# Kernel tuning notes

Measured on AMD Instinct MI355X. Metric: run time of the kernel, lower is better.

The kernel has to match this reference:

```python
import jax, jax.numpy as jnp
import numpy as np
import math

D_K = 64
ROUNDS = 4
BUCKET_LEN = 64


def _l2norm(x, axis):
    n = jnp.sqrt(jnp.sum(x * x, axis=axis, keepdims=True))
    return x / jnp.maximum(n, 1e-12)


def _look_back(x):
    # x: (B, n_buckets, bucket_len, ...) -> (B, n_buckets, 2*bucket_len, ...)
    # each bucket is concatenated with the previous bucket (wrapping at 0)
    shift = jnp.concatenate([x[:, -1:], x[:, :-1]], axis=1)
    return jnp.concatenate([shift, x], axis=2)


def _lsh_hash(query, rand_matrix):
    # returns position-tagged hashes: bucket_id * L + position, shape (B, L, R)
    B, L, D = query.shape
    qn = _l2norm(query, -1)
    rm = _l2norm(rand_matrix, 1)  # normalize over d_k dim, as in torch code
    xR = jnp.einsum('bld,bdrn->blrn', qn, rm)
    h = jnp.argmax(jnp.concatenate([xR, -xR], axis=-1), axis=-1).astype(jnp.int32)
    return h * L + jnp.arange(L, dtype=jnp.int32)[None, :, None]


def _attend(query, value, hash_indice, original_indice, sorted_hashes):
    B, L, D = query.shape
    nb = L // BUCKET_LEN
    R = ROUNDS
    # gather queries into hash-sorted order, per round: (B, L, D, R)
    rq = jnp.take_along_axis(query[:, :, :, None], hash_indice[:, :, None, :], axis=1)
    rq = rq.reshape(B, nb, BUCKET_LEN, D, R)
    lk = _l2norm(_look_back(rq), -2)  # keys = normalized lookback queries (shared QK)
    qk = jnp.einsum('bnijk,bnljk->bnilk', rq, lk) / math.sqrt(D_K)  # (B,nb,bl,2bl,R)
    # mask cross-bucket pairs
    sh = (sorted_hashes // L).reshape(B, nb, BUCKET_LEN, R)
    qk = jnp.where(sh[..., None, :] != _look_back(sh)[..., None, :, :], -1e9, qk)
    # mask self-attention (causal=False so no causal mask)
    qi = hash_indice.reshape(B, nb, BUCKET_LEN, R).astype(jnp.int32)
    ki = _look_back(qi)
    qk = jnp.where(qi[..., None, :] == ki[..., None, :, :], -1e5, qk)
    qk = qk.reshape(B, L, 2 * BUCKET_LEN, R)
    lse = jax.scipy.special.logsumexp(qk, axis=2)  # (B, L, R)
    p = jnp.exp(qk - lse[:, :, None, :]).reshape(B, nb, BUCKET_LEN, 2 * BUCKET_LEN, R)
    # gather values into sorted order and apply lookback attention
    rv = jnp.take_along_axis(value[:, :, :, None], hash_indice[:, :, None, :], axis=1)
    rv = rv.reshape(B, nb, BUCKET_LEN, D, R)
    att = jnp.einsum('bnijl,bnjkl->bnikl', p, _look_back(rv)).reshape(B, L, D, R)
    # scatter back to original order
    att = jnp.take_along_axis(att, original_indice[:, :, None, :], axis=1)
    lse = jnp.take_along_axis(lse, original_indice, axis=1)
    # NOTE: faithful to source, softmax over dim=1 (sequence dim)
    w = jax.nn.softmax(lse, axis=1)  # (B, L, R)
    return jnp.einsum('blir,blr->bli', att, w)  # (B, L, D)


def setup_inputs() -> dict:
    key = jax.random.key(0)
    k1, k2, k3 = jax.random.split(key, 3)
    B, L, D = 16, 8192, D_K
    n_buckets = L // BUCKET_LEN
    return {
        'query': jax.random.normal(k1, (B, L, D), jnp.float32),
        'value': jax.random.normal(k2, (B, L, D), jnp.float32),
        'rand_matrix': jax.random.normal(k3, (B, D, ROUNDS, n_buckets // 2), jnp.float32),
    }


def reference(query, value, rand_matrix):
    hashes = _lsh_hash(query, rand_matrix)          # (B, L, R) int32
    hash_indice = jnp.argsort(hashes, axis=1)       # sort positions by hash
    sorted_hashes = jnp.take_along_axis(hashes, hash_indice, axis=1)
    original_indice = jnp.argsort(hash_indice, axis=1)  # inverse permutation
    return _attend(query, value, hash_indice.astype(jnp.int32),
                   original_indice.astype(jnp.int32), sorted_hashes)
```

## Files before the change

kernel.cpp:

```cpp
#include <hip/hip_runtime.h>
#include <math.h>

#define B_   16
#define L_   8192
#define D_   64
#define R_   4
#define NB_  128
#define NH_  64

__device__ __forceinline__ float dpp_xor1(float x) {
    return __int_as_float(__builtin_amdgcn_mov_dpp(__float_as_int(x), 0xB1, 0xf, 0xf, true));
}
__device__ __forceinline__ float dpp_xor2(float x) {
    return __int_as_float(__builtin_amdgcn_mov_dpp(__float_as_int(x), 0x4E, 0xf, 0xf, true));
}
__device__ __forceinline__ float quad_bcast0(float x) {
    return __int_as_float(__builtin_amdgcn_mov_dpp(__float_as_int(x), 0x00, 0xf, 0xf, true));
}
__device__ __forceinline__ float quad_bcast1(float x) {
    return __int_as_float(__builtin_amdgcn_mov_dpp(__float_as_int(x), 0x55, 0xf, 0xf, true));
}
__device__ __forceinline__ float quad_bcast2(float x) {
    return __int_as_float(__builtin_amdgcn_mov_dpp(__float_as_int(x), 0xAA, 0xf, 0xf, true));
}
__device__ __forceinline__ float quad_bcast3(float x) {
    return __int_as_float(__builtin_amdgcn_mov_dpp(__float_as_int(x), 0xFF, 0xf, 0xf, true));
}

__global__ __launch_bounds__(64) void k_rmnorm(const float* __restrict__ rm, double* __restrict__ rmn) {
    int b = blockIdx.x >> 2, r = blockIdx.x & 3;
    int n = threadIdx.x;
    float v[D_];
    double ss = 0.0;
    #pragma unroll
    for (int d = 0; d < D_; ++d) {
        float f = rm[((size_t)(b * D_ + d) * R_ + r) * NH_ + n];
        v[d] = f;
        ss += (double)f * (double)f;
    }
    double nrm = sqrt(ss); if (nrm < 1e-12) nrm = 1e-12;
    double inv = 1.0 / nrm;
    double* o = rmn + ((size_t)(b * R_ + r) * NH_ + n) * D_;
    #pragma unroll
    for (int d = 0; d < D_; ++d) o[d] = (double)v[d] * inv;
}

__global__ __launch_bounds__(256) void k_hash(const float* __restrict__ q, const double* __restrict__ rmn,
                                              float* __restrict__ rn, int* __restrict__ h) {
    __shared__ double rms[NH_ * D_];
    int b = blockIdx.z, r = blockIdx.y;
    int l = blockIdx.x * 256 + threadIdx.x;
    const double* src = rmn + (size_t)(b * R_ + r) * NH_ * D_;
    for (int i = threadIdx.x; i < NH_ * D_; i += 256) rms[i] = src[i];
    const float* qp = q + ((size_t)b * L_ + l) * D_;
    double qd[D_];
    double ss = 0.0;
    #pragma unroll
    for (int d = 0; d < D_; d += 4) {
        float4 f = *(const float4*)(qp + d);
        qd[d] = f.x; qd[d+1] = f.y; qd[d+2] = f.z; qd[d+3] = f.w;
        ss += (double)f.x * f.x + (double)f.y * f.y + (double)f.z * f.z + (double)f.w * f.w;
    }
    __syncthreads();
    double best = -1.0e300; int bi = 0;
    for (int n = 0; n < NH_; ++n) {
        const double* kp = &rms[n * D_];
        double a0 = 0, a1 = 0, a2 = 0, a3 = 0;
        #pragma unroll
        for (int d = 0; d < D_; d += 4) {
            a0 = fma(qd[d],   kp[d],   a0);
            a1 = fma(qd[d+1], kp[d+1], a1);
            a2 = fma(qd[d+2], kp[d+2], a2);
            a3 = fma(qd[d+3], kp[d+3], a3);
        }
        double s = (a0 + a1) + (a2 + a3);
        if (s > best)  { best = s;  bi = n; }
        if (-s > best) { best = -s; bi = n + NH_; }
    }
    h[(size_t)(b * R_ + r) * L_ + l] = bi;
    if (r == 0) {
        double nrm = sqrt(ss); if (nrm < 1e-12) nrm = 1e-12;
        rn[(size_t)b * L_ + l] = (float)(1.0 / nrm);
    }
}

__global__ __launch_bounds__(64) void k_sort(const int* __restrict__ h, int* __restrict__ idx,
                                             int* __restrict__ sb, int* __restrict__ iv) {
    __shared__ unsigned int cnt[NB_ * 64];
    int br = blockIdx.x;
    const int* hh = h + (size_t)br * L_;
    int t = threadIdx.x;
    for (int i = t; i < NB_ * 64; i += 64) cnt[i] = 0;
    __syncthreads();
    int base = t * 128;
    for (int i = 0; i < 128; ++i) { int bk = hh[base + i]; cnt[bk * 64 + t]++; }
    __syncthreads();
    int fb = t * 128;
    unsigned int local = 0;
    for (int i = 0; i < 128; ++i) local += cnt[fb + i];
    unsigned int v = local;
    #pragma unroll
    for (int off = 1; off < 64; off <<= 1) {
        unsigned int u = __shfl_up(v, off);
        if (t >= off) v += u;
    }
    unsigned int run = v - local;
    for (int i = 0; i < 128; ++i) { unsigned int c0 = cnt[fb + i]; cnt[fb + i] = run; run += c0; }
    __syncthreads();
    int* oi = idx + (size_t)br * L_;
    int* ob = sb  + (size_t)br * L_;
    int* ivp = iv + (size_t)br * L_;
    for (int i = 0; i < 128; ++i) {
        int l = base + i; int bk = hh[l];
        unsigned int pos = cnt[bk * 64 + t]++;
        oi[pos] = l; ob[pos] = bk; ivp[l] = (int)pos;
    }
}

__global__ __launch_bounds__(64, 2) void k_flash(const float* __restrict__ q, const float* __restrict__ val,
                                                 const int* __restrict__ idx, const int* __restrict__ sb,
                                                 const float* __restrict__ rn, float* __restrict__ lse,
                                                 const float* __restrict__ gm, const float* __restrict__ gs,
                                                 float* __restrict__ out, float* __restrict__ contrib,
                                                 int r_fixed, int omode) {
    __shared__ float kt[16 * 80];
    __shared__ float vt[16 * 80];
    __shared__ int   kqs[16];
    __shared__ int   kbs[16];
    __shared__ float krs[16];
    int c = blockIdx.x, b = blockIdx.z;
    int r = (r_fixed < 0) ? (int)blockIdx.y : r_fixed;
    size_t sbase = (size_t)(b * R_ + r) * L_;
    int tid = threadIdx.x;
    int h = tid & 3;
    int posq = c * 64 + (tid >> 2) * 4;
    int mls[4];
    #pragma unroll
    for (int qq = 0; qq < 4; ++qq) mls[qq] = idx[sbase + posq + qq];
    int ownpos  = posq + h;
    int myl_own = idx[sbase + ownpos];
    int mybk_own = sb[sbase + ownpos];
    const float* qb = q   + (size_t)b * L_ * D_;
    const float* vb = val + (size_t)b * L_ * D_;
    float qv[4][16];
    #pragma unroll
    for (int qq = 0; qq < 4; ++qq) {
        const float* qp = qb + (size_t)mls[qq] * D_ + h * 16;
        #pragma unroll
        for (int i = 0; i < 16; i += 4) {
            float4 f = *(const float4*)(qp + i);
            qv[qq][i] = f.x; qv[qq][i+1] = f.y; qv[qq][i+2] = f.z; qv[qq][i+3] = f.w;
        }
    }
    float m = -3.0e38f, sum = 0.0f;
    float acc[4][16];
    #pragma unroll
    for (int qq = 0; qq < 4; ++qq)
        #pragma unroll
        for (int i = 0; i < 16; ++i) acc[qq][i] = 0.0f;

    #pragma unroll 1
    for (int s = 0; s < 8; ++s) {
        int ck = ((c + NB_ - 1 + (s >> 2)) & (NB_ - 1)) * 64 + (s & 3) * 16;
        __syncthreads();
        {
            int rw = tid >> 2, cc = tid & 3;
            int kl = idx[sbase + ck + rw];
            const float* kp = qb + (size_t)kl * D_ + cc * 16;
            float* kd = &kt[rw * 80 + cc * 20];
            #pragma unroll
            for (int i = 0; i < 16; i += 4) *(float4*)(kd + i) = *(const float4*)(kp + i);
            if (omode != 2) {
                const float* vp = vb + (size_t)kl * D_ + cc * 16;
                float* vd = &vt[rw * 80 + cc * 20];
                #pragma unroll
                for (int i = 0; i < 16; i += 4) *(float4*)(vd + i) = *(const float4*)(vp + i);
            }
            if (tid < 16) {
                int kl2 = idx[sbase + ck + tid];
                kqs[tid] = kl2;
                kbs[tid] = sb[sbase + ck + tid];
                krs[tid] = rn[(size_t)b * L_ + kl2];
            }
        }
        __syncthreads();
        float sc[16];
        #pragma unroll
        for (int j = 0; j < 16; ++j) {
            const float* kpj = &kt[j * 80 + h * 20];
            float p0 = 0, p1 = 0, p2 = 0, p3 = 0;
            #pragma unroll
            for (int i = 0; i < 16; i += 4) {
                float4 kk = *(const float4*)(kpj + i);
                p0 = fmaf(qv[0][i], kk.x, p0); p0 = fmaf(qv[0][i+1], kk.y, p0);
                p0 = fmaf(qv[0][i+2], kk.z, p0); p0 = fmaf(qv[0][i+3], kk.w, p0);
                p1 = fmaf(qv[1][i], kk.x, p1); p1 = fmaf(qv[1][i+1], kk.y, p1);
                p1 = fmaf(qv[1][i+2], kk.z, p1); p1 = fmaf(qv[1][i+3], kk.w, p1);
                p2 = fmaf(qv[2][i], kk.x, p2); p2 = fmaf(qv[2][i+1], kk.y, p2);
                p2 = fmaf(qv[2][i+2], kk.z, p2); p2 = fmaf(qv[2][i+3], kk.w, p2);
                p3 = fmaf(qv[3][i], kk.x, p3); p3 = fmaf(qv[3][i+1], kk.y, p3);
                p3 = fmaf(qv[3][i+2], kk.z, p3); p3 = fmaf(qv[3][i+3], kk.w, p3);
            }
            bool b0 = (h & 1), b1 = (h & 2) != 0;
            float u0 = b0 ? p1 : p0;
            float t0 = b0 ? p0 : p1;
            u0 += dpp_xor1(t0);
            float u2 = b0 ? p3 : p2;
            float t2 = b0 ? p2 : p3;
            u2 += dpp_xor1(t2);
            float dot = b1 ? u2 : u0;
            float t3 = b1 ? u0 : u2;
            dot += dpp_xor2(t3);
            float v2 = dot * krs[j] * 0.125f;
            v2 = (kbs[j] == mybk_own) ? v2 : -1.0e9f;
            if (kqs[j] == myl_own) v2 = -1.0e5f;
            sc[j] = v2;
        }
        float M = sc[0];
        #pragma unroll
        for (int j = 1; j < 16; ++j) M = fmaxf(M, sc[j]);
        float mn = fmaxf(m, M);
        float alpha = expf(m - mn);
        float ps = 0.0f;
        #pragma unroll
        for (int j = 0; j < 16; ++j) { sc[j] = expf(sc[j] - mn); ps += sc[j]; }
        sum = fmaf(sum, alpha, ps);
        m = mn;
        if (omode != 2) {
            float al0 = quad_bcast0(alpha), al1 = quad_bcast1(alpha);
            float al2 = quad_bcast2(alpha), al3 = quad_bcast3(alpha);
            #pragma unroll
            for (int i = 0; i < 16; ++i) {
                acc[0][i] *= al0; acc[1][i] *= al1; acc[2][i] *= al2; acc[3][i] *= al3;
            }
            #pragma unroll
            for (int j = 0; j < 16; ++j) {
                float pq0 = quad_bcast0(sc[j]), pq1 = quad_bcast1(sc[j]);
                float pq2 = quad_bcast2(sc[j]), pq3 = quad_bcast3(sc[j]);
                const float* vpj = &vt[j * 80 + h * 20];
                #pragma unroll
                for (int i = 0; i < 16; i += 4) {
                    float4 vv = *(const float4*)(vpj + i);
                    acc[0][i]   = fmaf(pq0, vv.x, acc[0][i]);   acc[0][i+1] = fmaf(pq0, vv.y, acc[0][i+1]);
                    acc[0][i+2] = fmaf(pq0, vv.z, acc[0][i+2]); acc[0][i+3] = fmaf(pq0, vv.w, acc[0][i+3]);
                    acc[1][i]   = fmaf(pq1, vv.x, acc[1][i]);   acc[1][i+1] = fmaf(pq1, vv.y, acc[1][i+1]);
                    acc[1][i+2] = fmaf(pq1, vv.z, acc[1][i+2]); acc[1][i+3] = fmaf(pq1, vv.w, acc[1][i+3]);
                    acc[2][i]   = fmaf(pq2, vv.x, acc[2][i]);   acc[2][i+1] = fmaf(pq2, vv.y, acc[2][i+1]);
                    acc[2][i+2] = fmaf(pq2, vv.z, acc[2][i+2]); acc[2][i+3] = fmaf(pq2, vv.w, acc[2][i+3]);
                    acc[3][i]   = fmaf(pq3, vv.x, acc[3][i]);   acc[3][i+1] = fmaf(pq3, vv.y, acc[3][i+1]);
                    acc[3][i+2] = fmaf(pq3, vv.z, acc[3][i+2]); acc[3][i+3] = fmaf(pq3, vv.w, acc[3][i+3]);
                }
            }
        }
    }
    float lse_own = m + logf(sum);
    if (omode != 3) lse[sbase + ownpos] = lse_own;
    if (omode == 0 || omode == 1) {
        float s0 = quad_bcast0(sum), s1 = quad_bcast1(sum), s2 = quad_bcast2(sum), s3 = quad_bcast3(sum);
        float iv0 = 1.0f / s0, iv1 = 1.0f / s1, iv2 = 1.0f / s2, iv3 = 1.0f / s3;
        float ivs[4] = {iv0, iv1, iv2, iv3};
        float* cbase = contrib + ((omode == 0) ? (size_t)(b * R_ + r) * L_ : (size_t)b * L_) * D_;
        #pragma unroll
        for (int qq = 0; qq < 4; ++qq) {
            float* cp = cbase + (size_t)(posq + qq) * D_ + h * 16;
            #pragma unroll
            for (int i = 0; i < 16; i += 4) {
                float4 o;
                o.x = acc[qq][i] * ivs[qq];   o.y = acc[qq][i+1] * ivs[qq];
                o.z = acc[qq][i+2] * ivs[qq]; o.w = acc[qq][i+3] * ivs[qq];
                *(float4*)(cp + i) = o;
            }
        }
    } else if (omode == 3) {
        int brr = b * R_ + r;
        float gmv = gm[brr], gsv = gs[brr];
        float l0 = quad_bcast0(lse_own), l1 = quad_bcast1(lse_own);
        float l2 = quad_bcast2(lse_own), l3 = quad_bcast3(lse_own);
        float s0 = quad_bcast0(sum), s1 = quad_bcast1(sum), s2 = quad_bcast2(sum), s3 = quad_bcast3(sum);
        float ws[4];
        ws[0] = expf(l0 - gmv) * gsv / s0; ws[1] = expf(l1 - gmv) * gsv / s1;
        ws[2] = expf(l2 - gmv) * gsv / s2; ws[3] = expf(l3 - gmv) * gsv / s3;
        #pragma unroll
        for (int qq = 0; qq < 4; ++qq) {
            float* op = out + ((size_t)b * L_ + mls[qq]) * D_ + h * 16;
            #pragma unroll
            for (int i = 0; i < 16; ++i) unsafeAtomicAdd(op + i, ws[qq] * acc[qq][i]);
        }
    }
}

__global__ __launch_bounds__(256) void k_wred(const float* __restrict__ lse, float* __restrict__ gm,
                                              float* __restrict__ gs, int r_w) {
    __shared__ float  sm[4];
    __shared__ double sd[4];
    int br = (r_w < 0) ? (int)blockIdx.x : ((int)blockIdx.x * R_ + r_w);
    const float* x = lse + (size_t)br * L_;
    int t = threadIdx.x;
    float mx = -3.0e38f;
    for (int i = t; i < L_; i += 256) mx = fmaxf(mx, x[i]);
    #pragma unroll
    for (int o = 32; o; o >>= 1) mx = fmaxf(mx, __shfl_down(mx, o));
    if ((t & 63) == 0) sm[t >> 6] = mx;
    __syncthreads();
    mx = fmaxf(fmaxf(sm[0], sm[1]), fmaxf(sm[2], sm[3]));
    double s = 0.0;
    for (int i = t; i < L_; i += 256) s += exp((double)x[i] - (double)mx);
    #pragma unroll
    for (int o = 32; o; o >>= 1) s += __shfl_down(s, o);
    if ((t & 63) == 0) sd[t >> 6] = s;
    __syncthreads();
    if (t == 0) { gm[br] = mx; gs[br] = (float)(1.0 / (sd[0] + sd[1] + sd[2] + sd[3])); }
}

__global__ __launch_bounds__(256) void k_comb_full(const float* __restrict__ contrib,
                                                   const int* __restrict__ iv,
                                                   const float* __restrict__ lse,
                                                   const float* __restrict__ gm,
                                                   const float* __restrict__ gs,
                                                   float* __restrict__ out) {
    int gid = blockIdx.x * 256 + threadIdx.x;
    int row = gid >> 2;
    int ch  = (gid & 3) * 16;
    int b = row >> 13, l = row & (L_ - 1);
    float s[16];
    #pragma unroll
    for (int i = 0; i < 16; ++i) s[i] = 0.0f;
    #pragma unroll
    for (int r = 0; r < R_; ++r) {
        int brr = b * R_ + r;
        int pos = iv[(size_t)brr * L_ + l];
        float w = expf(lse[(size_t)brr * L_ + pos] - gm[brr]) * gs[brr];
        const float* cp = contrib + ((size_t)brr * L_ + pos) * D_ + ch;
        #pragma unroll
        for (int i = 0; i < 16; i += 4) {
            float4 f = *(const float4*)(cp + i);
            s[i]   = fmaf(w, f.x, s[i]);   s[i+1] = fmaf(w, f.y, s[i+1]);
            s[i+2] = fmaf(w, f.z, s[i+2]); s[i+3] = fmaf(w, f.w, s[i+3]);
        }
    }
    float* op = out + (size_t)row * D_ + ch;
    #pragma unroll
    for (int i = 0; i < 16; i += 4) {
        float4 o; o.x = s[i]; o.y = s[i+1]; o.z = s[i+2]; o.w = s[i+3];
        *(float4*)(op + i) = o;
    }
}

__global__ __launch_bounds__(256) void k_comb_add(const float* __restrict__ contrib,
                                                  const int* __restrict__ iv,
                                                  const float* __restrict__ lse,
                                                  const float* __restrict__ gm,
                                                  const float* __restrict__ gs,
                                                  float* __restrict__ out, int r) {
    int gid = blockIdx.x * 256 + threadIdx.x;
    int row = gid >> 2;
    int ch  = (gid & 3) * 16;
    int b = row >> 13, l = row & (L_ - 1);
    int brr = b * R_ + r;
    int pos = iv[(size_t)brr * L_ + l];
    float w = expf(lse[(size_t)brr * L_ + pos] - gm[brr]) * gs[brr];
    const float* cp = contrib + ((size_t)b * L_ + pos) * D_ + ch;
    float* op = out + (size_t)row * D_ + ch;
    #pragma unroll
    for (int i = 0; i < 16; i += 4) {
        float4 f = *(const float4*)(cp + i);
        float4 o = *(const float4*)(op + i);
        o.x = fmaf(w, f.x, o.x); o.y = fmaf(w, f.y, o.y);
        o.z = fmaf(w, f.z, o.z); o.w = fmaf(w, f.w, o.w);
        *(float4*)(op + i) = o;
    }
}

#define OFF_RMN     0u
#define OFF_RN      2097152u
#define OFF_H       2621440u
#define OFF_IDX     4718592u
#define OFF_SB      6815744u
#define OFF_LSE     8912896u
#define OFF_GM      11010048u
#define OFF_GS      11010304u
#define OFF_INV     11010560u
#define OFF_CONTRIB 13107712u
#define CONTRIB_FULL_BYTES  134217728ull
#define CONTRIB_SLICE_BYTES 33554432ull

extern "C" void kernel_launch(void* const* d_in, const int* in_sizes, int n_in,
                              void* d_out, int out_size, void* d_ws, size_t ws_size,
                              hipStream_t stream) {
    const float* q  = (const float*)d_in[0];
    const float* v  = (const float*)d_in[1];
    const float* rm = (const float*)d_in[2];
    float* out = (float*)d_out;
    char* ws = (char*)d_ws;
    double* rmn = (double*)(ws + OFF_RMN);
    float*  rn  = (float*)(ws + OFF_RN);
    int*    h   = (int*)(ws + OFF_H);
    int*    idx = (int*)(ws + OFF_IDX);
    int*    sb  = (int*)(ws + OFF_SB);
    float*  lse = (float*)(ws + OFF_LSE);
    float*  gm  = (float*)(ws + OFF_GM);
    float*  gs  = (float*)(ws + OFF_GS);
    int*    iv  = (int*)(ws + OFF_INV);
    float*  contrib = (float*)(ws + OFF_CONTRIB);

    int tierA = (ws_size >= (size_t)OFF_CONTRIB + CONTRIB_FULL_BYTES) ? 1 : 0;
    int tierB = (!tierA && ws_size >= (size_t)OFF_CONTRIB + CONTRIB_SLICE_BYTES) ? 1 : 0;

    hipLaunchKernelGGL(k_rmnorm, dim3(B_ * R_), dim3(64), 0, stream, rm, rmn);
    hipLaunchKernelGGL(k_hash, dim3(L_ / 256, R_, B_), dim3(256), 0, stream, q, rmn, rn, h);
    hipLaunchKernelGGL(k_sort, dim3(B_ * R_), dim3(64), 0, stream, h, idx, sb, iv);

    if (tierA) {
        hipLaunchKernelGGL(k_flash, dim3(NB_, R_, B_), dim3(64), 0, stream, q, v, idx, sb, rn,
                           lse, gm, gs, out, contrib, -1, 0);
        hipLaunchKernelGGL(k_wred, dim3(B_ * R_), dim3(256), 0, stream, lse, gm, gs, -1);
        hipLaunchKernelGGL(k_comb_full, dim3(B_ * L_ * 4 / 256), dim3(256), 0, stream,
                           contrib, iv, lse, gm, gs, out);
    } else if (tierB) {
        hipMemsetAsync(d_out, 0, (size_t)B_ * L_ * D_ * sizeof(float), stream);
        for (int r = 0; r < R_; ++r) {
            hipLaunchKernelGGL(k_flash, dim3(NB_, 1, B_), dim3(64), 0, stream, q, v, idx, sb, rn,
                               lse, gm, gs, out, contrib, r, 1);
            hipLaunchKernelGGL(k_wred, dim3(B_), dim3(256), 0, stream, lse, gm, gs, r);
            hipLaunchKernelGGL(k_comb_add, dim3(B_ * L_ * 4 / 256), dim3(256), 0, stream,
                               contrib, iv, lse, gm, gs, out, r);
        }
    } else {
        hipMemsetAsync(d_out, 0, (size_t)B_ * L_ * D_ * sizeof(float), stream);
        hipLaunchKernelGGL(k_flash, dim3(NB_, R_, B_), dim3(64), 0, stream, q, v, idx, sb, rn,
                           lse, gm, gs, out, contrib, -1, 2);
        hipLaunchKernelGGL(k_wred, dim3(B_ * R_), dim3(256), 0, stream, lse, gm, gs, -1);
        hipLaunchKernelGGL(k_flash, dim3(NB_, R_, B_), dim3(64), 0, stream, q, v, idx, sb, rn,
                           lse, gm, gs, out, contrib, -1, 3);
    }
}
```

Measured before the change: 648.1 us.

## Use fp32 hashing with fp64 fallback and fixed-max softmax in attention

```diff
diff --git a/kernel.cpp b/kernel.cpp
--- a/kernel.cpp
+++ b/kernel.cpp
@@ -47,35 +47,64 @@
 
 __global__ __launch_bounds__(256) void k_hash(const float* __restrict__ q, const double* __restrict__ rmn,
                                               float* __restrict__ rn, int* __restrict__ h) {
-    __shared__ double rms[NH_ * D_];
+    __shared__ double rmd[NH_ * D_];
+    __shared__ float  rms[NH_ * D_];
     int b = blockIdx.z, r = blockIdx.y;
     int l = blockIdx.x * 256 + threadIdx.x;
     const double* src = rmn + (size_t)(b * R_ + r) * NH_ * D_;
-    for (int i = threadIdx.x; i < NH_ * D_; i += 256) rms[i] = src[i];
+    for (int i = threadIdx.x; i < NH_ * D_; i += 256) {
+        double dv = src[i];
+        rmd[i] = dv;
+        rms[i] = (float)dv;
+    }
     const float* qp = q + ((size_t)b * L_ + l) * D_;
-    double qd[D_];
+    float qf[D_];
     double ss = 0.0;
     #pragma unroll
     for (int d = 0; d < D_; d += 4) {
         float4 f = *(const float4*)(qp + d);
-        qd[d] = f.x; qd[d+1] = f.y; qd[d+2] = f.z; qd[d+3] = f.w;
+        qf[d] = f.x; qf[d+1] = f.y; qf[d+2] = f.z; qf[d+3] = f.w;
         ss += (double)f.x * f.x + (double)f.y * f.y + (double)f.z * f.z + (double)f.w * f.w;
     }
     __syncthreads();
-    double best = -1.0e300; int bi = 0;
+    float best = -1.0e30f, second = -1.0e30f; int bi = 0;
     for (int n = 0; n < NH_; ++n) {
-        const double* kp = &rms[n * D_];
-        double a0 = 0, a1 = 0, a2 = 0, a3 = 0;
+        const float* kp = &rms[n * D_];
+        float a0 = 0, a1 = 0, a2 = 0, a3 = 0;
         #pragma unroll
         for (int d = 0; d < D_; d += 4) {
-            a0 = fma(qd[d],   kp[d],   a0);
-            a1 = fma(qd[d+1], kp[d+1], a1);
-            a2 = fma(qd[d+2], kp[d+2], a2);
-            a3 = fma(qd[d+3], kp[d+3], a3);
-        }
-        double s = (a0 + a1) + (a2 + a3);
-        if (s > best)  { best = s;  bi = n; }
-        if (-s > best) { best = -s; bi = n + NH_; }
+            a0 = fmaf(qf[d],   kp[d],   a0);
+            a1 = fmaf(qf[d+1], kp[d+1], a1);
+            a2 = fmaf(qf[d+2], kp[d+2], a2);
+            a3 = fmaf(qf[d+3], kp[d+3], a3);
+        }
+        float s = (a0 + a1) + (a2 + a3);
+        if (s > best)       { second = best; best = s; bi = n; }
+        else if (s > second)  second = s;
+        float ns = -s;
+        if (ns > best)      { second = best; best = ns; bi = n + NH_; }
+        else if (ns > second) second = ns;
+    }
+    float qn = (float)sqrt(ss);
+    if (best - second < 3.0e-5f * qn + 1.0e-7f) {
+        double qd[D_];
+        #pragma unroll
+        for (int d = 0; d < D_; ++d) qd[d] = (double)qf[d];
+        double bestd = -1.0e300; bi = 0;
+        for (int n = 0; n < NH_; ++n) {
+            const double* kp = &rmd[n * D_];
+            double a0 = 0, a1 = 0, a2 = 0, a3 = 0;
+            #pragma unroll
+            for (int d = 0; d < D_; d += 4) {
+                a0 = fma(qd[d],   kp[d],   a0);
+                a1 = fma(qd[d+1], kp[d+1], a1);
+                a2 = fma(qd[d+2], kp[d+2], a2);
+                a3 = fma(qd[d+3], kp[d+3], a3);
+            }
+            double s = (a0 + a1) + (a2 + a3);
+            if (s > bestd)  { bestd = s;  bi = n; }
+            if (-s > bestd) { bestd = -s; bi = n + NH_; }
+        }
     }
     h[(size_t)(b * R_ + r) * L_ + l] = bi;
     if (r == 0) {
@@ -140,6 +169,7 @@
     int ownpos  = posq + h;
     int myl_own = idx[sbase + ownpos];
     int mybk_own = sb[sbase + ownpos];
+    float m_own = 0.125f / rn[(size_t)b * L_ + myl_own];
     const float* qb = q   + (size_t)b * L_ * D_;
     const float* vb = val + (size_t)b * L_ * D_;
     float qv[4][16];
@@ -152,7 +182,7 @@
             qv[qq][i] = f.x; qv[qq][i+1] = f.y; qv[qq][i+2] = f.z; qv[qq][i+3] = f.w;
         }
     }
-    float m = -3.0e38f, sum = 0.0f;
+    float ps[4] = {0.0f, 0.0f, 0.0f, 0.0f};
     float acc[4][16];
     #pragma unroll
     for (int qq = 0; qq < 4; ++qq)
@@ -180,11 +210,10 @@
                 int kl2 = idx[sbase + ck + tid];
                 kqs[tid] = kl2;
                 kbs[tid] = sb[sbase + ck + tid];
-                krs[tid] = rn[(size_t)b * L_ + kl2];
+                krs[tid] = rn[(size_t)b * L_ + kl2] * 0.125f;
             }
         }
         __syncthreads();
-        float sc[16];
         #pragma unroll
         for (int j = 0; j < 16; ++j) {
             const float* kpj = &kt[j * 80 + h * 20];
@@ -211,32 +240,14 @@
             float dot = b1 ? u2 : u0;
             float t3 = b1 ? u0 : u2;
             dot += dpp_xor2(t3);
-            float v2 = dot * krs[j] * 0.125f;
-            v2 = (kbs[j] == mybk_own) ? v2 : -1.0e9f;
-            if (kqs[j] == myl_own) v2 = -1.0e5f;
-            sc[j] = v2;
-        }
-        float M = sc[0];
-        #pragma unroll
-        for (int j = 1; j < 16; ++j) M = fmaxf(M, sc[j]);
-        float mn = fmaxf(m, M);
-        float alpha = expf(m - mn);
-        float ps = 0.0f;
-        #pragma unroll
-        for (int j = 0; j < 16; ++j) { sc[j] = expf(sc[j] - mn); ps += sc[j]; }
-        sum = fmaf(sum, alpha, ps);
-        m = mn;
-        if (omode != 2) {
-            float al0 = quad_bcast0(alpha), al1 = quad_bcast1(alpha);
-            float al2 = quad_bcast2(alpha), al3 = quad_bcast3(alpha);
-            #pragma unroll
-            for (int i = 0; i < 16; ++i) {
-                acc[0][i] *= al0; acc[1][i] *= al1; acc[2][i] *= al2; acc[3][i] *= al3;
-            }
-            #pragma unroll
-            for (int j = 0; j < 16; ++j) {
-                float pq0 = quad_bcast0(sc[j]), pq1 = quad_bcast1(sc[j]);
-                float pq2 = quad_bcast2(sc[j]), pq3 = quad_bcast3(sc[j]);
+            float sc = dot * krs[j];
+            sc = (kbs[j] == mybk_own) ? sc : -1.0e9f;
+            if (kqs[j] == myl_own) sc = -1.0e5f;
+            float p = __expf(sc - m_own);
+            ps[j & 3] += p;
+            if (omode != 2) {
+                float pq0 = quad_bcast0(p), pq1 = quad_bcast1(p);
+                float pq2 = quad_bcast2(p), pq3 = quad_bcast3(p);
                 const float* vpj = &vt[j * 80 + h * 20];
                 #pragma unroll
                 for (int i = 0; i < 16; i += 4) {
@@ -253,12 +264,15 @@
             }
         }
     }
-    float lse_own = m + logf(sum);
+    float sum = (ps[0] + ps[1]) + (ps[2] + ps[3]);
+    float lse_own, inv_own;
+    if (sum > 0.0f) { lse_own = m_own + logf(sum); inv_own = 1.0f / sum; }
+    else            { lse_own = -3.0e38f;          inv_own = 0.0f; }
     if (omode != 3) lse[sbase + ownpos] = lse_own;
     if (omode == 0 || omode == 1) {
-        float s0 = quad_bcast0(sum), s1 = quad_bcast1(sum), s2 = quad_bcast2(sum), s3 = quad_bcast3(sum);
-        float iv0 = 1.0f / s0, iv1 = 1.0f / s1, iv2 = 1.0f / s2, iv3 = 1.0f / s3;
-        float ivs[4] = {iv0, iv1, iv2, iv3};
+        float ivs[4];
+        ivs[0] = quad_bcast0(inv_own); ivs[1] = quad_bcast1(inv_own);
+        ivs[2] = quad_bcast2(inv_own); ivs[3] = quad_bcast3(inv_own);
         float* cbase = contrib + ((omode == 0) ? (size_t)(b * R_ + r) * L_ : (size_t)b * L_) * D_;
         #pragma unroll
         for (int qq = 0; qq < 4; ++qq) {
@@ -274,17 +288,17 @@
     } else if (omode == 3) {
         int brr = b * R_ + r;
         float gmv = gm[brr], gsv = gs[brr];
-        float l0 = quad_bcast0(lse_own), l1 = quad_bcast1(lse_own);
-        float l2 = quad_bcast2(lse_own), l3 = quad_bcast3(lse_own);
-        float s0 = quad_bcast0(sum), s1 = quad_bcast1(sum), s2 = quad_bcast2(sum), s3 = quad_bcast3(sum);
-        float ws[4];
-        ws[0] = expf(l0 - gmv) * gsv / s0; ws[1] = expf(l1 - gmv) * gsv / s1;
-        ws[2] = expf(l2 - gmv) * gsv / s2; ws[3] = expf(l3 - gmv) * gsv / s3;
+        float ls4[4], iv4[4];
+        ls4[0] = quad_bcast0(lse_own); ls4[1] = quad_bcast1(lse_own);
+        ls4[2] = quad_bcast2(lse_own); ls4[3] = quad_bcast3(lse_own);
+        iv4[0] = quad_bcast0(inv_own); iv4[1] = quad_bcast1(inv_own);
+        iv4[2] = quad_bcast2(inv_own); iv4[3] = quad_bcast3(inv_own);
         #pragma unroll
         for (int qq = 0; qq < 4; ++qq) {
+            float w = __expf(ls4[qq] - gmv) * gsv * iv4[qq];
             float* op = out + ((size_t)b * L_ + mls[qq]) * D_ + h * 16;
             #pragma unroll
-            for (int i = 0; i < 16; ++i) unsafeAtomicAdd(op + i, ws[qq] * acc[qq][i]);
+            for (int i = 0; i < 16; ++i) unsafeAtomicAdd(op + i, w * acc[qq][i]);
         }
     }
 }
```

After: 617.5 us. 1.05x faster.
